# Optimization experiments

Measured on AMD Instinct MI355X. Metric: run time of the kernel, lower is better.

Reference implementation:

```python
import jax, jax.numpy as jnp
import numpy as np

N_NODES = 100000
N_EDGES = 1600000
EMB_DIM = 128
BN_EPS = 1e-5


def setup_inputs() -> dict:
    key = jax.random.key(0)
    k = jax.random.split(key, 5)
    x = jax.random.normal(k[0], (N_NODES, EMB_DIM), dtype=jnp.float32)
    src = jax.random.randint(k[1], (N_EDGES,), 0, N_NODES)
    dst = jax.random.randint(k[2], (N_EDGES,), 0, N_NODES)
    W = jax.random.normal(k[3], (EMB_DIM, EMB_DIM), dtype=jnp.float32) / np.float32(np.sqrt(EMB_DIM))
    b = jnp.zeros((EMB_DIM,), dtype=jnp.float32)
    gamma = jnp.ones((EMB_DIM,), dtype=jnp.float32)
    beta = jnp.zeros((EMB_DIM,), dtype=jnp.float32)
    return {"x": x, "src": src, "dst": dst, "W": W, "b": b, "gamma": gamma, "beta": beta}


def reference(x, src, dst, W, b, gamma, beta):
    n = x.shape[0]
    ones = jnp.ones(src.shape, dtype=x.dtype)
    # DGL GraphConv norm='both': degrees clamped to min 1
    deg_out = jnp.maximum(jax.ops.segment_sum(ones, src, num_segments=n), 1.0)
    deg_in = jnp.maximum(jax.ops.segment_sum(ones, dst, num_segments=n), 1.0)
    norm_src = jax.lax.rsqrt(deg_out)  # [N]
    norm_dst = jax.lax.rsqrt(deg_in)   # [N]
    # W applied before aggregation (in_feats == out_feats path in DGL)
    h = (x * norm_src[:, None]) @ W                              # [N, D]
    agg = jax.ops.segment_sum(h[src], dst, num_segments=n)       # SpMM gather/scatter, [N, D]
    h = agg * norm_dst[:, None] + b                              # [N, D]
    # BatchNorm1d over nodes (training-mode batch stats, biased variance)
    mean = jnp.mean(h, axis=0)
    var = jnp.var(h, axis=0)
    h = (h - mean) * jax.lax.rsqrt(var + BN_EPS) * gamma + beta
    h = jax.nn.relu(h)
    # dropout: identity in eval-mode reference
    return h + x  # residual
```

## Files before the change

### kernel.cpp

```cpp
#include <hip/hip_runtime.h>
#include <hip/hip_bf16.h>

#define NN 100000
#define NE 1600000
#define D  128
#define BN_EPS 1e-5f

#define CB  782
#define NC  256
#define EPC (NE / NC)
#define NSLICE  2
#define SLICESZ 61600
#define SW      (SLICESZ / 4)
#define SCH     256
#define EPH (NE / SCH)

typedef __attribute__((ext_vector_type(8))) short bf16x8;
typedef __attribute__((ext_vector_type(4))) float f32x4;

#define WLD 136

static __device__ __forceinline__ ushort f2bf(float f) {
    __hip_bfloat16 b = __float2bfloat16(f);
    return *reinterpret_cast<ushort*>(&b);
}
static __device__ __forceinline__ float bflo(unsigned v) {
    return __uint_as_float((v & 0xffffu) << 16);
}
static __device__ __forceinline__ float bfhi(unsigned v) {
    return __uint_as_float(v & 0xffff0000u);
}

__global__ __launch_bounds__(256) void k_front(const int* __restrict__ src,
                                               const int* __restrict__ dst,
                                               const float* __restrict__ W,
                                               ushort* __restrict__ WT,
                                               int* __restrict__ SP,
                                               int* __restrict__ P,
                                               float* __restrict__ stats) {
    __shared__ int hist[SW];
    __shared__ int dh[CB];
    const int t = threadIdx.x;
    const int s = blockIdx.x >> 8;
    const int c = blockIdx.x & 255;
    for (int i = t; i < SW; i += 256) hist[i] = 0;
    for (int i = t; i < CB; i += 256) dh[i] = 0;
    __syncthreads();

    const int lo = s * SLICESZ;
    const int base = c * EPH;
    for (int i = t; i < EPH; i += 256) {
        int k = src[base + i] - lo;
        if ((unsigned)k < (unsigned)SLICESZ)
            atomicAdd(&hist[k >> 2], 1 << ((k & 3) * 8));
    }
    if (s == 0) {
        for (int i = t; i < EPH; i += 256)
            atomicAdd(&dh[dst[base + i] >> 7], 1);
    }
    __syncthreads();

    int* outS = SP + (size_t)blockIdx.x * SW;
    for (int i = t; i < SW; i += 256) outS[i] = hist[i];
    if (s == 0)
        for (int i = t; i < CB; i += 256) P[i * NC + c] = dh[i];
    if (s == 1 && c < 64) {
        int i = c * 256 + t;
        int n = i >> 7, k2 = i & 127;
        WT[i] = f2bf(W[k2 * D + n]);
    }
    if (s == 1 && c == 64) stats[t] = 0.0f;
}


__global__ __launch_bounds__(256) void k_cscanA(int* __restrict__ P,
                                                int* __restrict__ bintotal) {
    __shared__ int sh[NC];
    const int b = blockIdx.x;
    const int t = threadIdx.x;
    const int v = P[b * NC + t];
    sh[t] = v;
    __syncthreads();
    for (int off = 1; off < NC; off <<= 1) {
        int u = (t >= off) ? sh[t - off] : 0;
        __syncthreads();
        sh[t] += u;
        __syncthreads();
    }
    P[b * NC + t] = sh[t] - v;
    if (t == NC - 1) bintotal[b] = sh[t];
}

__global__ __launch_bounds__(1024) void k_cscanB(const int* __restrict__ bintotal,
                                                 int* __restrict__ binbase) {
    __shared__ int sh[1024];
    const int t = threadIdx.x;
    const int v = (t < CB) ? bintotal[t] : 0;
    sh[t] = v;
    __syncthreads();
    for (int off = 1; off < 1024; off <<= 1) {
        int u = (t >= off) ? sh[t - off] : 0;
        __syncthreads();
        sh[t] += u;
        __syncthreads();
    }
    if (t < CB) binbase[t] = sh[t] - v;
    if (t == CB - 1) binbase[CB] = sh[t];
}

__global__ __launch_bounds__(256) void k_cscatter(const int* __restrict__ dst,
                                                  const int* __restrict__ src,
                                                  const int* __restrict__ P,
                                                  const int* __restrict__ binbase,
                                                  int* __restrict__ sedge) {
    __shared__ int cur[CB];
    const int c = blockIdx.x;
    const int t = threadIdx.x;
    for (int i = t; i < CB; i += 256) cur[i] = binbase[i] + P[i * NC + c];
    __syncthreads();
    const int base = c * EPC;
    for (int i = t; i < EPC; i += 256) {
        int d = dst[base + i];
        int pos = atomicAdd(&cur[d >> 7], 1);
        sedge[pos] = src[base + i] | ((d & 127) << 17);
    }
}

__global__ __launch_bounds__(256) void k_fine(const int* __restrict__ sedge,
                                              const int* __restrict__ binbase,
                                              int* __restrict__ ptr,
                                              int* __restrict__ esrc) {
    __shared__ int fh[128], fp[128], fcur[128];
    const int b = blockIdx.x;
    const int t = threadIdx.x;
    const int lo = binbase[b], hi = binbase[b + 1];
    if (t < 128) fh[t] = 0;
    __syncthreads();
    for (int i = lo + t; i < hi; i += 256)
        atomicAdd(&fh[(unsigned)sedge[i] >> 17], 1);
    __syncthreads();
    if (t < 128) fp[t] = fh[t];
    __syncthreads();
    for (int off = 1; off < 128; off <<= 1) {
        int u = (t < 128 && t >= off) ? fp[t - off] : 0;
        __syncthreads();
        if (t < 128) fp[t] += u;
        __syncthreads();
    }
    if (t < 128) {
        const int node = b * 128 + t;
        const int ex = fp[t] - fh[t];
        fcur[t] = ex;
        if (node < NN) {
            ptr[node] = lo + ex;
        } else if (node == NN) {
            ptr[NN] = lo + ex;
        }
    }
    __syncthreads();
    for (int i = lo + t; i < hi; i += 256) {
        unsigned v = (unsigned)sedge[i];
        int pos = atomicAdd(&fcur[v >> 17], 1);
        esrc[lo + pos] = v & 0x1FFFF;
    }
}


__global__ void k_smerge(const int* __restrict__ SP, float* __restrict__ degout) {
    int w = blockIdx.x * 256 + threadIdx.x;
    if (w >= NSLICE * SW) return;
    const int s = w / SW, wi = w - s * SW;
    const int n0 = s * SLICESZ + wi * 4;
    if (n0 >= NN) return;
    const int* col = SP + (size_t)s * SCH * SW + wi;
    int b0 = 0, b1 = 0, b2 = 0, b3 = 0;
#pragma unroll 8
    for (int c = 0; c < SCH; ++c) {
        unsigned v = (unsigned)col[(size_t)c * SW];
        b0 += v & 0xFF;
        b1 += (v >> 8) & 0xFF;
        b2 += (v >> 16) & 0xFF;
        b3 += (v >> 24);
    }
    degout[n0] = (float)b0;
    if (n0 + 1 < NN) degout[n0 + 1] = (float)b1;
    if (n0 + 2 < NN) degout[n0 + 2] = (float)b2;
    if (n0 + 3 < NN) degout[n0 + 3] = (float)b3;
}

__global__ __launch_bounds__(256) void k_gemm(const float* __restrict__ x,
                                              const float* __restrict__ degout,
                                              const ushort* __restrict__ WT,
                                              ushort* __restrict__ h) {
    __shared__ ushort Wl[D * WLD];

    const int t = threadIdx.x;
    for (int s = t; s < 2048; s += 256) {
        int row = s >> 4, slot = s & 15;
        uint4 v = *reinterpret_cast<const uint4*>(WT + row * D + slot * 8);
        *reinterpret_cast<uint4*>(&Wl[row * WLD + slot * 8]) = v;
    }
    __syncthreads();

    const int wave = t >> 6;
    const int lane = t & 63;
    const int m16  = lane & 15;
    const int kq   = lane >> 4;
    const int row  = blockIdx.x * 64 + wave * 16 + m16;
    const int rc   = row < NN ? row : NN - 1;

    const float nrm = rsqrtf(fmaxf(degout[rc], 1.0f));

    bf16x8 afrag[4];
    const float* xr = x + (size_t)rc * D + kq * 8;
#pragma unroll
    for (int kt = 0; kt < 4; ++kt) {
        f32x4 lo = *reinterpret_cast<const f32x4*>(xr + kt * 32);
        f32x4 hi = *reinterpret_cast<const f32x4*>(xr + kt * 32 + 4);
        union { bf16x8 v; ushort u[8]; } af;
#pragma unroll
        for (int j = 0; j < 4; ++j) {
            af.u[j]     = f2bf(lo[j] * nrm);
            af.u[4 + j] = f2bf(hi[j] * nrm);
        }
        afrag[kt] = af.v;
    }

    f32x4 acc[8];
#pragma unroll
    for (int nt = 0; nt < 8; ++nt) acc[nt] = (f32x4)(0.0f);

#pragma unroll
    for (int kt = 0; kt < 4; ++kt) {
#pragma unroll
        for (int nt = 0; nt < 8; ++nt) {
            int n = nt * 16 + m16;
            const bf16x8 bfrag = *reinterpret_cast<const bf16x8*>(
                &Wl[n * WLD + kt * 32 + kq * 8]);
            acc[nt] = __builtin_amdgcn_mfma_f32_16x16x32_bf16(afrag[kt], bfrag, acc[nt], 0, 0, 0);
        }
    }

    const int orow = blockIdx.x * 64 + wave * 16 + kq * 4;
#pragma unroll
    for (int nt = 0; nt < 8; ++nt) {
#pragma unroll
        for (int r = 0; r < 4; ++r) {
            int rr = orow + r;
            if (rr < NN) h[(size_t)rr * D + nt * 16 + m16] = f2bf(acc[nt][r]);
        }
    }
}

__global__ __launch_bounds__(256) void k_agg(const ushort* __restrict__ h,
                                             const int* __restrict__ ptr,
                                             const int* __restrict__ esrc,
                                             const float* __restrict__ b,
                                             ushort* __restrict__ h2) {
    const int node = blockIdx.x * 4 + (threadIdx.x >> 6);
    const int lane = threadIdx.x & 63;
    if (node >= NN) return;
    const int s0 = ptr[node];
    const int s1 = ptr[node + 1];
    const int eg = lane >> 4;
    const int cb = (lane & 15) * 8;

    float acc[8];
#pragma unroll
    for (int j = 0; j < 8; ++j) acc[j] = 0.0f;

    for (int i = s0; i < s1; i += 16) {
        int  idx[4];
        bool p[4];
        uint4 v[4];
#pragma unroll
        for (int u = 0; u < 4; ++u) {
            int ii = i + eg + 4 * u;
            p[u] = ii < s1;
            if (p[u]) idx[u] = esrc[ii];
        }
#pragma unroll
        for (int u = 0; u < 4; ++u)
            if (p[u]) v[u] = *reinterpret_cast<const uint4*>(h + (size_t)idx[u] * D + cb);
#pragma unroll
        for (int u = 0; u < 4; ++u) {
            if (p[u]) {
                acc[0] += bflo(v[u].x); acc[1] += bfhi(v[u].x);
                acc[2] += bflo(v[u].y); acc[3] += bfhi(v[u].y);
                acc[4] += bflo(v[u].z); acc[5] += bfhi(v[u].z);
                acc[6] += bflo(v[u].w); acc[7] += bfhi(v[u].w);
            }
        }
    }
#pragma unroll
    for (int j = 0; j < 8; ++j) {
        acc[j] += __shfl_xor(acc[j], 16, 64);
        acc[j] += __shfl_xor(acc[j], 32, 64);
    }
    if (eg == 0) {
        const float nrm = rsqrtf(fmaxf((float)(s1 - s0), 1.0f));
        uint4 o;
        unsigned w[4];
#pragma unroll
        for (int m = 0; m < 4; ++m) {
            float e0 = acc[2 * m]     * nrm + b[cb + 2 * m];
            float e1 = acc[2 * m + 1] * nrm + b[cb + 2 * m + 1];
            w[m] = (unsigned)f2bf(e0) | ((unsigned)f2bf(e1) << 16);
        }
        o.x = w[0]; o.y = w[1]; o.z = w[2]; o.w = w[3];
        *reinterpret_cast<uint4*>(h2 + (size_t)node * D + cb) = o;
    }
}

__global__ __launch_bounds__(256) void k_stats(const unsigned* __restrict__ h2u,
                                               float* __restrict__ stats) {
    __shared__ float red[4][256];
    const int t = threadIdx.x;
    float s1lo = 0.f, s1hi = 0.f, s2lo = 0.f, s2hi = 0.f;
    const int total = NN * (D / 2);
    const int stride = gridDim.x * 256;
    for (int i = blockIdx.x * 256 + t; i < total; i += stride) {
        unsigned v = h2u[i];
        float lo = bflo(v), hi = bfhi(v);
        s1lo += lo; s1hi += hi;
        s2lo += lo * lo; s2hi += hi * hi;
    }
    red[0][t] = s1lo; red[1][t] = s1hi; red[2][t] = s2lo; red[3][t] = s2hi;
    __syncthreads();
    if (t < 64) {
        const int c = t * 2;
        float a0 = red[0][t] + red[0][t + 64] + red[0][t + 128] + red[0][t + 192];
        float a1 = red[1][t] + red[1][t + 64] + red[1][t + 128] + red[1][t + 192];
        float q0 = red[2][t] + red[2][t + 64] + red[2][t + 128] + red[2][t + 192];
        float q1 = red[3][t] + red[3][t + 64] + red[3][t + 128] + red[3][t + 192];
        atomicAdd(&stats[c], a0);
        atomicAdd(&stats[c + 1], a1);
        atomicAdd(&stats[128 + c], q0);
        atomicAdd(&stats[128 + c + 1], q1);
    }
}

__global__ void k_final(const uint2* __restrict__ h2v, const float4* __restrict__ xv,
                        const float* __restrict__ gamma, const float* __restrict__ beta,
                        const float* __restrict__ stats, float4* __restrict__ outv) {
    const int i = blockIdx.x * 256 + threadIdx.x;
    const int total = NN * (D / 4);
    if (i >= total) return;
    const int c = (i & 31) * 4;
    const float inv_n = 1.0f / (float)NN;
    uint2 v = h2v[i];
    float4 xx = xv[i];
    float hv[4] = { bflo(v.x), bfhi(v.x), bflo(v.y), bfhi(v.y) };
    float xr[4] = { xx.x, xx.y, xx.z, xx.w };
    float o[4];
#pragma unroll
    for (int m = 0; m < 4; ++m) {
        float mean = stats[c + m] * inv_n;
        float var  = stats[128 + c + m] * inv_n - mean * mean;
        float t = (hv[m] - mean) * rsqrtf(var + BN_EPS) * gamma[c + m] + beta[c + m];
        o[m] = fmaxf(t, 0.0f) + xr[m];
    }
    float4 ov; ov.x = o[0]; ov.y = o[1]; ov.z = o[2]; ov.w = o[3];
    outv[i] = ov;
}

extern "C" void kernel_launch(void* const* d_in, const int* in_sizes, int n_in,
                              void* d_out, int out_size, void* d_ws, size_t ws_size,
                              hipStream_t stream) {
    const float* x     = (const float*)d_in[0];
    const int*   src   = (const int*)d_in[1];
    const int*   dst   = (const int*)d_in[2];
    const float* W     = (const float*)d_in[3];
    const float* b     = (const float*)d_in[4];
    const float* gamma = (const float*)d_in[5];
    const float* beta  = (const float*)d_in[6];
    float* out = (float*)d_out;

    float* ws     = (float*)d_ws;
    ushort* h2    = (ushort*)ws;
    float* degout = ws + (size_t)NN * D;
    float* stats  = degout + NN;
    int*   ptr    = (int*)(stats + 256);
    int*   esrc   = ptr + (NN + 1);
    ushort* WT    = (ushort*)(esrc + NE);

    int* sedge    = (int*)ws;
    int* SP       = sedge + NE;
    int* P        = SP + (size_t)NSLICE * SCH * SW;
    int* bintotal = P + (size_t)CB * NC;
    int* binbase  = bintotal + CB;

    ushort* h = (ushort*)d_out;

    k_front<<<NSLICE * SCH, 256, 0, stream>>>(src, dst, W, WT, SP, P, stats);
    k_cscanA<<<CB, 256, 0, stream>>>(P, bintotal);
    k_cscanB<<<1, 1024, 0, stream>>>(bintotal, binbase);
    k_cscatter<<<NC, 256, 0, stream>>>(dst, src, P, binbase, sedge);
    k_smerge<<<(NSLICE * SW + 255) / 256, 256, 0, stream>>>(SP, degout);
    k_gemm<<<(NN + 63) / 64, 256, 0, stream>>>(x, degout, WT, h);
    k_fine<<<CB, 256, 0, stream>>>(sedge, binbase, ptr, esrc);
    k_agg<<<(NN + 3) / 4, 256, 0, stream>>>(h, ptr, esrc, b, h2);
    k_stats<<<1024, 256, 0, stream>>>((const unsigned*)h2, stats);
    k_final<<<(NN * (D / 4) + 255) / 256, 256, 0, stream>>>((const uint2*)h2, (const float4*)x,
                                                            gamma, beta, stats, (float4*)out);
}
```

Measured before the change: 231.8 us.

## Merge independent kernels via block-index dispatch to cut launch count

Combines the column scan with the degree merge into one launch, and the dense GEMM with the fine CSR bucketing into another, choosing the branch by block index. This removes two kernel launches and lets independent work overlap on the device. The GEMM blocks now carry the fine-stage shared arrays, and the fine-stage blocks reserve the GEMM's large W tile in shared memory, which may reduce occupancy for the fine-stage blocks.

```diff
diff --git a/kernel.cpp b/kernel.cpp
--- a/kernel.cpp
+++ b/kernel.cpp
@@ -14,6 +14,9 @@
 #define SW      (SLICESZ / 4)
 #define SCH     256
 #define EPH (NE / SCH)
+
+#define GB   ((NN + 63) / 64)
+#define SMB  ((NSLICE * SW + 255) / 256)
 
 typedef __attribute__((ext_vector_type(8))) short bf16x8;
 typedef __attribute__((ext_vector_type(4))) float f32x4;
@@ -72,23 +75,46 @@
     if (s == 1 && c == 64) stats[t] = 0.0f;
 }
 
-
-__global__ __launch_bounds__(256) void k_cscanA(int* __restrict__ P,
-                                                int* __restrict__ bintotal) {
-    __shared__ int sh[NC];
-    const int b = blockIdx.x;
-    const int t = threadIdx.x;
-    const int v = P[b * NC + t];
-    sh[t] = v;
-    __syncthreads();
-    for (int off = 1; off < NC; off <<= 1) {
-        int u = (t >= off) ? sh[t - off] : 0;
-        __syncthreads();
-        sh[t] += u;
-        __syncthreads();
-    }
-    P[b * NC + t] = sh[t] - v;
-    if (t == NC - 1) bintotal[b] = sh[t];
+__global__ __launch_bounds__(256) void k_mid(int* __restrict__ P,
+                                             int* __restrict__ bintotal,
+                                             const int* __restrict__ SP,
+                                             float* __restrict__ degout) {
+    const int t = threadIdx.x;
+    if (blockIdx.x < CB) {
+        __shared__ int sh[NC];
+        const int b = blockIdx.x;
+        const int v = P[b * NC + t];
+        sh[t] = v;
+        __syncthreads();
+        for (int off = 1; off < NC; off <<= 1) {
+            int u = (t >= off) ? sh[t - off] : 0;
+            __syncthreads();
+            sh[t] += u;
+            __syncthreads();
+        }
+        P[b * NC + t] = sh[t] - v;
+        if (t == NC - 1) bintotal[b] = sh[t];
+    } else {
+        int w = (blockIdx.x - CB) * 256 + t;
+        if (w >= NSLICE * SW) return;
+        const int s = w / SW, wi = w - s * SW;
+        const int n0 = s * SLICESZ + wi * 4;
+        if (n0 >= NN) return;
+        const int* col = SP + (size_t)s * SCH * SW + wi;
+        int b0 = 0, b1 = 0, b2 = 0, b3 = 0;
+#pragma unroll 8
+        for (int c = 0; c < SCH; ++c) {
+            unsigned v = (unsigned)col[(size_t)c * SW];
+            b0 += v & 0xFF;
+            b1 += (v >> 8) & 0xFF;
+            b2 += (v >> 16) & 0xFF;
+            b3 += (v >> 24);
+        }
+        degout[n0] = (float)b0;
+        if (n0 + 1 < NN) degout[n0 + 1] = (float)b1;
+        if (n0 + 2 < NN) degout[n0 + 2] = (float)b2;
+        if (n0 + 3 < NN) degout[n0 + 3] = (float)b3;
+    }
 }
 
 __global__ __launch_bounds__(1024) void k_cscanB(const int* __restrict__ bintotal,
@@ -126,128 +152,105 @@
     }
 }
 
-__global__ __launch_bounds__(256) void k_fine(const int* __restrict__ sedge,
-                                              const int* __restrict__ binbase,
-                                              int* __restrict__ ptr,
-                                              int* __restrict__ esrc) {
+__global__ __launch_bounds__(256) void k_gf(const float* __restrict__ x,
+                                            const float* __restrict__ degout,
+                                            const ushort* __restrict__ WT,
+                                            ushort* __restrict__ h,
+                                            const int* __restrict__ sedge,
+                                            const int* __restrict__ binbase,
+                                            int* __restrict__ ptr,
+                                            int* __restrict__ esrc) {
+    __shared__ ushort Wl[D * WLD];
     __shared__ int fh[128], fp[128], fcur[128];
-    const int b = blockIdx.x;
-    const int t = threadIdx.x;
-    const int lo = binbase[b], hi = binbase[b + 1];
-    if (t < 128) fh[t] = 0;
-    __syncthreads();
-    for (int i = lo + t; i < hi; i += 256)
-        atomicAdd(&fh[(unsigned)sedge[i] >> 17], 1);
-    __syncthreads();
-    if (t < 128) fp[t] = fh[t];
-    __syncthreads();
-    for (int off = 1; off < 128; off <<= 1) {
-        int u = (t < 128 && t >= off) ? fp[t - off] : 0;
-        __syncthreads();
-        if (t < 128) fp[t] += u;
-        __syncthreads();
-    }
-    if (t < 128) {
-        const int node = b * 128 + t;
-        const int ex = fp[t] - fh[t];
-        fcur[t] = ex;
-        if (node < NN) {
-            ptr[node] = lo + ex;
-        } else if (node == NN) {
-            ptr[NN] = lo + ex;
-        }
-    }
-    __syncthreads();
-    for (int i = lo + t; i < hi; i += 256) {
-        unsigned v = (unsigned)sedge[i];
-        int pos = atomicAdd(&fcur[v >> 17], 1);
-        esrc[lo + pos] = v & 0x1FFFF;
-    }
-}
-
-
-__global__ void k_smerge(const int* __restrict__ SP, float* __restrict__ degout) {
-    int w = blockIdx.x * 256 + threadIdx.x;
-    if (w >= NSLICE * SW) return;
-    const int s = w / SW, wi = w - s * SW;
-    const int n0 = s * SLICESZ + wi * 4;
-    if (n0 >= NN) return;
-    const int* col = SP + (size_t)s * SCH * SW + wi;
-    int b0 = 0, b1 = 0, b2 = 0, b3 = 0;
-#pragma unroll 8
-    for (int c = 0; c < SCH; ++c) {
-        unsigned v = (unsigned)col[(size_t)c * SW];
-        b0 += v & 0xFF;
-        b1 += (v >> 8) & 0xFF;
-        b2 += (v >> 16) & 0xFF;
-        b3 += (v >> 24);
-    }
-    degout[n0] = (float)b0;
-    if (n0 + 1 < NN) degout[n0 + 1] = (float)b1;
-    if (n0 + 2 < NN) degout[n0 + 2] = (float)b2;
-    if (n0 + 3 < NN) degout[n0 + 3] = (float)b3;
-}
-
-__global__ __launch_bounds__(256) void k_gemm(const float* __restrict__ x,
-                                              const float* __restrict__ degout,
-                                              const ushort* __restrict__ WT,
-                                              ushort* __restrict__ h) {
-    __shared__ ushort Wl[D * WLD];
-
-    const int t = threadIdx.x;
-    for (int s = t; s < 2048; s += 256) {
-        int row = s >> 4, slot = s & 15;
-        uint4 v = *reinterpret_cast<const uint4*>(WT + row * D + slot * 8);
-        *reinterpret_cast<uint4*>(&Wl[row * WLD + slot * 8]) = v;
-    }
-    __syncthreads();
-
-    const int wave = t >> 6;
-    const int lane = t & 63;
-    const int m16  = lane & 15;
-    const int kq   = lane >> 4;
-    const int row  = blockIdx.x * 64 + wave * 16 + m16;
-    const int rc   = row < NN ? row : NN - 1;
-
-    const float nrm = rsqrtf(fmaxf(degout[rc], 1.0f));
-
-    bf16x8 afrag[4];
-    const float* xr = x + (size_t)rc * D + kq * 8;
-#pragma unroll
-    for (int kt = 0; kt < 4; ++kt) {
-        f32x4 lo = *reinterpret_cast<const f32x4*>(xr + kt * 32);
-        f32x4 hi = *reinterpret_cast<const f32x4*>(xr + kt * 32 + 4);
-        union { bf16x8 v; ushort u[8]; } af;
-#pragma unroll
-        for (int j = 0; j < 4; ++j) {
-            af.u[j]     = f2bf(lo[j] * nrm);
-            af.u[4 + j] = f2bf(hi[j] * nrm);
-        }
-        afrag[kt] = af.v;
-    }
-
-    f32x4 acc[8];
-#pragma unroll
-    for (int nt = 0; nt < 8; ++nt) acc[nt] = (f32x4)(0.0f);
-
-#pragma unroll
-    for (int kt = 0; kt < 4; ++kt) {
+    const int t = threadIdx.x;
+
+    if (blockIdx.x < GB) {
+        for (int s = t; s < 2048; s += 256) {
+            int row = s >> 4, slot = s & 15;
+            uint4 v = *reinterpret_cast<const uint4*>(WT + row * D + slot * 8);
+            *reinterpret_cast<uint4*>(&Wl[row * WLD + slot * 8]) = v;
+        }
+        __syncthreads();
+
+        const int wave = t >> 6;
+        const int lane = t & 63;
+        const int m16  = lane & 15;
+        const int kq   = lane >> 4;
+        const int row  = blockIdx.x * 64 + wave * 16 + m16;
+        const int rc   = row < NN ? row : NN - 1;
+
+        const float nrm = rsqrtf(fmaxf(degout[rc], 1.0f));
+
+        bf16x8 afrag[4];
+        const float* xr = x + (size_t)rc * D + kq * 8;
+#pragma unroll
+        for (int kt = 0; kt < 4; ++kt) {
+            f32x4 lo = *reinterpret_cast<const f32x4*>(xr + kt * 32);
+            f32x4 hi = *reinterpret_cast<const f32x4*>(xr + kt * 32 + 4);
+            union { bf16x8 v; ushort u[8]; } af;
+#pragma unroll
+            for (int j = 0; j < 4; ++j) {
+                af.u[j]     = f2bf(lo[j] * nrm);
+                af.u[4 + j] = f2bf(hi[j] * nrm);
+            }
+            afrag[kt] = af.v;
+        }
+
+        f32x4 acc[8];
+#pragma unroll
+        for (int nt = 0; nt < 8; ++nt) acc[nt] = (f32x4)(0.0f);
+
+#pragma unroll
+        for (int kt = 0; kt < 4; ++kt) {
+#pragma unroll
+            for (int nt = 0; nt < 8; ++nt) {
+                int n = nt * 16 + m16;
+                const bf16x8 bfrag = *reinterpret_cast<const bf16x8*>(
+                    &Wl[n * WLD + kt * 32 + kq * 8]);
+                acc[nt] = __builtin_amdgcn_mfma_f32_16x16x32_bf16(afrag[kt], bfrag, acc[nt], 0, 0, 0);
+            }
+        }
+
+        const int orow = blockIdx.x * 64 + wave * 16 + kq * 4;
 #pragma unroll
         for (int nt = 0; nt < 8; ++nt) {
-            int n = nt * 16 + m16;
-            const bf16x8 bfrag = *reinterpret_cast<const bf16x8*>(
-                &Wl[n * WLD + kt * 32 + kq * 8]);
-            acc[nt] = __builtin_amdgcn_mfma_f32_16x16x32_bf16(afrag[kt], bfrag, acc[nt], 0, 0, 0);
-        }
-    }
-
-    const int orow = blockIdx.x * 64 + wave * 16 + kq * 4;
-#pragma unroll
-    for (int nt = 0; nt < 8; ++nt) {
-#pragma unroll
-        for (int r = 0; r < 4; ++r) {
-            int rr = orow + r;
-            if (rr < NN) h[(size_t)rr * D + nt * 16 + m16] = f2bf(acc[nt][r]);
+#pragma unroll
+            for (int r = 0; r < 4; ++r) {
+                int rr = orow + r;
+                if (rr < NN) h[(size_t)rr * D + nt * 16 + m16] = f2bf(acc[nt][r]);
+            }
+        }
+    } else {
+        const int b = blockIdx.x - GB;
+        const int lo = binbase[b], hi = binbase[b + 1];
+        if (t < 128) fh[t] = 0;
+        __syncthreads();
+        for (int i = lo + t; i < hi; i += 256)
+            atomicAdd(&fh[(unsigned)sedge[i] >> 17], 1);
+        __syncthreads();
+        if (t < 128) fp[t] = fh[t];
+        __syncthreads();
+        for (int off = 1; off < 128; off <<= 1) {
+            int u = (t < 128 && t >= off) ? fp[t - off] : 0;
+            __syncthreads();
+            if (t < 128) fp[t] += u;
+            __syncthreads();
+        }
+        if (t < 128) {
+            const int node = b * 128 + t;
+            const int ex = fp[t] - fh[t];
+            fcur[t] = ex;
+            if (node < NN) {
+                ptr[node] = lo + ex;
+            } else if (node == NN) {
+                ptr[NN] = lo + ex;
+            }
+        }
+        __syncthreads();
+        for (int i = lo + t; i < hi; i += 256) {
+            unsigned v = (unsigned)sedge[i];
+            int pos = atomicAdd(&fcur[v >> 17], 1);
+            esrc[lo + pos] = v & 0x1FFFF;
         }
     }
 }
@@ -393,12 +396,10 @@
     ushort* h = (ushort*)d_out;
 
     k_front<<<NSLICE * SCH, 256, 0, stream>>>(src, dst, W, WT, SP, P, stats);
-    k_cscanA<<<CB, 256, 0, stream>>>(P, bintotal);
+    k_mid<<<CB + SMB, 256, 0, stream>>>(P, bintotal, SP, degout);
     k_cscanB<<<1, 1024, 0, stream>>>(bintotal, binbase);
     k_cscatter<<<NC, 256, 0, stream>>>(dst, src, P, binbase, sedge);
-    k_smerge<<<(NSLICE * SW + 255) / 256, 256, 0, stream>>>(SP, degout);
-    k_gemm<<<(NN + 63) / 64, 256, 0, stream>>>(x, degout, WT, h);
-    k_fine<<<CB, 256, 0, stream>>>(sedge, binbase, ptr, esrc);
+    k_gf<<<GB + CB, 256, 0, stream>>>(x, degout, WT, h, sedge, binbase, ptr, esrc);
     k_agg<<<(NN + 3) / 4, 256, 0, stream>>>(h, ptr, esrc, b, h2);
     k_stats<<<1024, 256, 0, stream>>>((const unsigned*)h2, stats);
     k_final<<<(NN * (D / 4) + 255) / 256, 256, 0, stream>>>((const uint2*)h2, (const float4*)x,
```

Result: faster. 226.2 us (-2.4%).
